# Performance work log

Hardware: AMD Instinct MI355X
Metric: run time of the kernel (lower is better)

## Reference

```python
import jax, jax.numpy as jnp
import numpy as np

NCLS = 21
HW = 41  # featUpsample target size


def setup_inputs() -> dict:
    key = jax.random.key(0)
    ks = jax.random.split(key, 8)
    x = jax.random.normal(ks[0], (4, 2048, 33, 33), dtype=jnp.float32)
    diffW = jax.random.uniform(ks[1], (4, HW * HW, HW * HW), dtype=jnp.float32)
    # conv weights init normal(0, 0.01) as in the torch module
    conv_w = jax.random.normal(ks[2], (1024, 2048, 3, 3), dtype=jnp.float32) * 0.01
    conv_b = jnp.zeros((1024,), jnp.float32)
    cls_w = jax.random.normal(ks[3], (NCLS, 1024, 1, 1), dtype=jnp.float32) * 0.01
    cls_b = jnp.zeros((NCLS,), jnp.float32)
    sm_scale_w = jnp.ones((1, NCLS), jnp.float32) * 1.5   # softMax_scale.weights
    pool_w = jnp.ones((1, NCLS), jnp.float32) * 5.0       # weiPooling.weights
    ms_scales = jnp.array([0.95, 0.75, 0.6, 0.4], jnp.float32)
    return {"x": x, "diffW": diffW, "conv_w": conv_w, "conv_b": conv_b,
            "cls_w": cls_w, "cls_b": cls_b, "sm_scale_w": sm_scale_w,
            "pool_w": pool_w, "ms_scales": ms_scales}


def reference(x, diffW, conv_w, conv_b, cls_w, cls_b, sm_scale_w, pool_w, ms_scales):
    bs = x.shape[0]
    # bilinear upsample to 41x41 (align_corners=False semantics, same as jax.image.resize)
    x = jax.image.resize(x, (bs, x.shape[1], HW, HW), method="bilinear")
    # ASPP branch 0: dilated 3x3 conv, dilation=padding=6 keeps 41x41
    feat = jax.lax.conv_general_dilated(
        x, conv_w, window_strides=(1, 1), padding=((6, 6), (6, 6)),
        rhs_dilation=(6, 6), dimension_numbers=("NCHW", "OIHW", "NCHW"))
    feat = feat + conv_b[None, :, None, None]          # [bs,1024,41,41]
    d = feat.shape[1]
    wh = HW * HW
    f2 = feat.reshape(bs, d, wh)                        # [bs,1024,wh]
    cw = cls_w.reshape(NCLS, d)                         # 1x1 conv weight

    logits = []
    for it in range(4):
        cs = (diffW > ms_scales[it]).astype(f2.dtype)   # [bs,wh,wh]
        # diag(1/rowsum) @ cs, then transpose -> column-normalized-after-transpose
        norm = (cs / cs.sum(axis=2, keepdims=True)).transpose(0, 2, 1)
        od = jnp.einsum("bdn,bnm->bdm", f2, norm)       # diffusion-smoothed features
        logits.append(jnp.einsum("bdm,cd->bcm", od, cw) + cls_b[None, :, None])
    wei_cum = jnp.stack(logits, axis=1)                 # [bs,4,ncls,wh]

    # softMax_scale: softmax over the scale (ns) axis of scaled logits
    wei_mask = jax.nn.softmax(sm_scale_w.reshape(1, 1, NCLS, 1) * wei_cum, axis=1)
    wei_cum2 = jax.nn.softmax((wei_cum * wei_mask).sum(axis=1), axis=1)  # [bs,ncls,wh]

    # weiPooling
    wei = jax.nn.softmax(wei_cum2, axis=1)
    w2 = jax.nn.softmax(wei * jnp.exp(pool_w[0]).reshape(1, NCLS, 1), axis=2)
    pooled = jnp.einsum("bcm,bdm->bcd", w2, f2)         # [bs,ncls,1024]

    # pred_sw with the 1x1 classifier weights
    out = (pooled * cw[None]).sum(axis=2) + cls_b[None]  # [bs,ncls]
    prob = jax.nn.sigmoid(out).reshape(bs, 1, NCLS)
    return (prob, wei_cum2, wei, wei_mask)
```

## Files before the change

### kernel.cpp

```cpp
#include <hip/hip_runtime.h>
#include <hip/hip_bf16.h>
#include <math.h>

#define NCLS 21
#define WH 1681
#define WHP 1684
#define BS 4
#define CIN 2048
#define NSRC 1089
#define KPOS 18432
#define MR 192
#define HS 836352
#define NT 53
#define NZ 8
#define PSLAB (16L * 22L * WHP)
#define MGK 16
#define MPOS 387072

typedef __attribute__((ext_vector_type(8))) __bf16 bf16x8;
typedef __attribute__((ext_vector_type(4))) float f32x4;

#define WS_W2M   0L
#define WS_KC    393216L
#define WS_H2    393248L
#define WS_WCUM  (WS_H2 + 4L * HS)
#define WS_G     (WS_WCUM + 564816L)
#define WS_GSW   (WS_G + 141204L)
#define WS_PACC0 (WS_GSW + 108544L)
#define WS_W2P   (WS_PACC0 + 591712L)
#define WS_W2MB  (WS_W2P + 6193152L)

static __device__ __forceinline__ unsigned short f2bf(float v) {
    unsigned int b = __float_as_uint(v);
    b += 0x7FFFu + ((b >> 16) & 1u);
    return (unsigned short)(b >> 16);
}


__global__ __launch_bounds__(128) void k_mergemm(const float* __restrict__ convw,
                                                 const float* __restrict__ clsw,
                                                 float* __restrict__ w2p) {
    int tid = threadIdx.x;
    int pos0 = blockIdx.x * 512 + tid * 4;
    int kz = blockIdx.y;
    int k0 = kz * 64;
    const float* cb = convw + (long)k0 * KPOS + pos0;

    float4 acc[21];
#pragma unroll
    for (int c = 0; c < 21; ++c) acc[c] = (float4){0.f, 0.f, 0.f, 0.f};

    float4 cur[4];
#pragma unroll
    for (int j = 0; j < 4; ++j) cur[j] = *(const float4*)(cb + (long)j * KPOS);

    for (int kk = 0; kk < 64; kk += 4) {
        float4 nxt[4];
        if (kk + 4 < 64) {
#pragma unroll
            for (int j = 0; j < 4; ++j) nxt[j] = *(const float4*)(cb + (long)(kk + 4 + j) * KPOS);
        }
        float4 cw[21];
#pragma unroll
        for (int c = 0; c < 21; ++c) cw[c] = *(const float4*)&clsw[c * 1024 + k0 + kk];
#pragma unroll
        for (int j = 0; j < 4; ++j) {
#pragma unroll
            for (int c = 0; c < 21; ++c) {
                float s = ((const float*)&cw[c])[j];
                acc[c].x += s * cur[j].x; acc[c].y += s * cur[j].y;
                acc[c].z += s * cur[j].z; acc[c].w += s * cur[j].w;
            }
        }
        if (kk + 4 < 64) {
#pragma unroll
            for (int j = 0; j < 4; ++j) cur[j] = nxt[j];
        }
    }
    float* op = w2p + (long)kz * MPOS + pos0;
#pragma unroll
    for (int c = 0; c < 21; ++c) *(float4*)(op + (long)c * KPOS) = acc[c];
}

__global__ void k_mfin(const float* __restrict__ w2p, float* __restrict__ w2m) {
    int gid = blockIdx.x * blockDim.x + threadIdx.x;
    if (gid >= MPOS) return;
    int r = gid / 2048;
    int i = gid - r * 2048;
    int c = r / 9, t = r - c * 9;
    long src = (long)c * KPOS + i * 9 + t;
    float s = 0.f;
#pragma unroll
    for (int kz = 0; kz < MGK; ++kz) s += w2p[(long)kz * MPOS + src];
    w2m[gid] = s;
}

__global__ void k_wpack(const float* __restrict__ w2m, unsigned short* __restrict__ w2mb) {
    int gid = blockIdx.x * blockDim.x + threadIdx.x;
    if (gid >= 64 * 12 * 64) return;
    int lane = gid & 63;
    int rt = (gid >> 6) % 12;
    int kc = gid / (64 * 12);
    int cl = lane & 15, kg = lane >> 4;
    const float* src = w2m + (long)(rt * 16 + cl) * 2048 + kc * 32 + kg * 8;
    unsigned short o[8];
#pragma unroll
    for (int j = 0; j < 8; ++j) o[j] = f2bf(src[j]);
    unsigned short* p = w2mb + (long)gid * 8;
#pragma unroll
    for (int j = 0; j < 8; ++j) p[j] = o[j];
}

__global__ void k_const(const float* __restrict__ clsw, const float* __restrict__ convb,
                        const float* __restrict__ clsb, float* __restrict__ Kc) {
    __shared__ float red[256];
    int c = blockIdx.x;
    float s = 0.f;
    for (int d = threadIdx.x; d < 1024; d += 256) s += clsw[c * 1024 + d] * convb[d];
    red[threadIdx.x] = s; __syncthreads();
    for (int o = 128; o > 0; o >>= 1) {
        if (threadIdx.x < o) red[threadIdx.x] += red[threadIdx.x + o];
        __syncthreads();
    }
    if (threadIdx.x == 0) Kc[c] = red[0] + clsb[c];
}

__global__ __launch_bounds__(256) void k_gemmm(const unsigned short* __restrict__ w2mb,
                                               const float* __restrict__ x,
                                               float* __restrict__ Hp) {
    __shared__ unsigned short Bs[2][64][40];
    int tid = threadIdx.x;
    int lane = tid & 63, wv = tid >> 6;
    int kg = lane >> 4, cl = lane & 15;
    int n0 = blockIdx.x * 64;
    int b  = blockIdx.y;
    int ks = blockIdx.z;

    const float* xb = x + ((long)b * CIN + ks * 512) * NSRC + n0 + lane;
    bool nok = (n0 + lane) < NSRC;

    f32x4 acc[3][4];
#pragma unroll
    for (int i = 0; i < 3; ++i)
#pragma unroll
        for (int ct = 0; ct < 4; ++ct) acc[i][ct] = (f32x4){0.f, 0.f, 0.f, 0.f};

    for (int ch = 0; ch < 16; ++ch) {
        const float* xc = xb + (long)(ch * 32 + wv * 8) * NSRC;
        float xr[8];
#pragma unroll
        for (int jj = 0; jj < 8; ++jj) xr[jj] = nok ? xc[(long)jj * NSRC] : 0.f;
        bf16x8 afr[3];
        const unsigned short* wb = w2mb + (((long)(ks * 16 + ch) * 12 + wv * 3) * 64 + lane) * 8;
#pragma unroll
        for (int i = 0; i < 3; ++i) afr[i] = *(const bf16x8*)(wb + (long)i * 64 * 8);
        union { unsigned short u[8]; bf16x8 v; } bw;
#pragma unroll
        for (int jj = 0; jj < 8; ++jj) bw.u[jj] = f2bf(xr[jj]);
        int buf = ch & 1;
        *(bf16x8*)&Bs[buf][lane][wv * 8] = bw.v;
        __syncthreads();
#pragma unroll
        for (int ct = 0; ct < 4; ++ct) {
            bf16x8 bf = *(const bf16x8*)&Bs[buf][ct * 16 + cl][kg * 8];
#pragma unroll
            for (int i = 0; i < 3; ++i)
                acc[i][ct] = __builtin_amdgcn_mfma_f32_16x16x32_bf16(afr[i], bf, acc[i][ct], 0, 0, 0);
        }
    }
    float* Hb = Hp + (long)ks * HS + (long)b * MR * NSRC;
#pragma unroll
    for (int i = 0; i < 3; ++i) {
        int r0 = (wv * 3 + i) * 16 + 4 * kg;
#pragma unroll
        for (int ct = 0; ct < 4; ++ct) {
            int n = n0 + ct * 16 + cl;
            if (n < NSRC) {
#pragma unroll
                for (int rr = 0; rr < 4; ++rr)
                    Hb[(long)(r0 + rr) * NSRC + n] = acc[i][ct][rr];
            }
        }
    }
}

__global__ void k_combine(const float* __restrict__ Hp, float* __restrict__ g) {
    int gid = blockIdx.x * blockDim.x + threadIdx.x;
    if (gid >= BS * NCLS * WH) return;
    int m = gid % WH;
    int t_ = gid / WH;
    int c = t_ % NCLS;
    int b = t_ / NCLS;
    int yy = m / 41, xx = m - yy * 41;
    const float S = 33.0f / 41.0f;
    int y0a[3], y1a[3], x0a[3], x1a[3];
    float wya[3], wxa[3];
    bool oky[3], okx[3];
#pragma unroll
    for (int o = 0; o < 3; ++o) {
        int yp = yy + 6 * o - 6;
        oky[o] = (yp >= 0 && yp < 41);
        float sy = (yp + 0.5f) * S - 0.5f;
        float fy = floorf(sy);
        wya[o] = sy - fy;
        int y0 = (int)fy;
        y0a[o] = min(max(y0, 0), 32);
        y1a[o] = min(max(y0 + 1, 0), 32);
        int xp = xx + 6 * o - 6;
        okx[o] = (xp >= 0 && xp < 41);
        float sx = (xp + 0.5f) * S - 0.5f;
        float fx = floorf(sx);
        wxa[o] = sx - fx;
        int x0 = (int)fx;
        x0a[o] = min(max(x0, 0), 32);
        x1a[o] = min(max(x0 + 1, 0), 32);
    }
    float acc = 0.f;
    const float* Hb = Hp + ((long)b * MR + c * 9) * NSRC;
#pragma unroll
    for (int ty = 0; ty < 3; ++ty) {
#pragma unroll
        for (int tx = 0; tx < 3; ++tx) {
            if (oky[ty] && okx[tx]) {
                const float* hr = Hb + (ty * 3 + tx) * NSRC;
                int i00 = y0a[ty] * 33 + x0a[tx], i01 = y0a[ty] * 33 + x1a[tx];
                int i10 = y1a[ty] * 33 + x0a[tx], i11 = y1a[ty] * 33 + x1a[tx];
                float v00 = 0.f, v01 = 0.f, v10 = 0.f, v11 = 0.f;
#pragma unroll
                for (int s = 0; s < 4; ++s) {
                    const float* h2 = hr + (long)s * HS;
                    v00 += h2[i00]; v01 += h2[i01]; v10 += h2[i10]; v11 += h2[i11];
                }
                float wy = wya[ty], wx = wxa[tx];
                float v0 = v00 + wx * (v01 - v00);
                float v1 = v10 + wx * (v11 - v10);
                acc += v0 + wy * (v1 - v0);
            }
        }
    }
    g[gid] = acc;
}

__global__ void k_gpack(const float* __restrict__ g, unsigned short* __restrict__ Gsw) {
    int gid = blockIdx.x * blockDim.x + threadIdx.x;
    if (gid >= BS * NT * 2 * 64) return;
    int lane = gid & 63;
    int t = gid >> 6;
    int ct = t & 1; t >>= 1;
    int nt = t % NT;
    int b  = t / NT;
    int col = ct * 16 + (lane & 15);
    int nb = nt * 32 + (lane >> 4) * 8;
    unsigned short out[8];
#pragma unroll
    for (int j = 0; j < 8; ++j) {
        int n = nb + j;
        unsigned short v = 0;
        if (n < WH) {
            if (col < NCLS) v = f2bf(g[((long)b * NCLS + col) * WH + n]);
            else if (col == NCLS) v = 0x3F80;
        }
        out[j] = v;
    }
    unsigned short* p = Gsw + (long)gid * 8;
#pragma unroll
    for (int j = 0; j < 8; ++j) p[j] = out[j];
}

__global__ __launch_bounds__(256) void k_dgemm(const float* __restrict__ diffW,
                                               const unsigned short* __restrict__ Gsw,
                                               const float* __restrict__ msc,
                                               float* __restrict__ pacc) {
    int tid  = threadIdx.x;
    int lane = tid & 63, wv = tid >> 6;
    int b = blockIdx.y, z = blockIdx.z;
    int m0w = blockIdx.x * 64 + wv * 16;
    int kg = lane >> 4;
    int cl = lane & 15;
    int mA = m0w + cl; if (mA > WH - 1) mA = WH - 1;
    float thr[4];
#pragma unroll
    for (int it = 0; it < 4; ++it) thr[it] = msc[it];
    int nt0 = (z * NT) / NZ;
    int nt1 = ((z + 1) * NT) / NZ;
    const float* drow = diffW + ((long)b * WH + mA) * WH;
    const unsigned short* gb = Gsw + (long)b * NT * 2 * 64 * 8;

    f32x4 accv[4][2];
#pragma unroll
    for (int it = 0; it < 4; ++it)
#pragma unroll
        for (int ct = 0; ct < 2; ++ct) accv[it][ct] = (f32x4){0.f, 0.f, 0.f, 0.f};

    for (int nt = nt0; nt < nt1; ++nt) {
        int nb = nt * 32 + kg * 8;
        float dw[8];
        if (nb + 7 <= WH - 1) {
#pragma unroll
            for (int j = 0; j < 8; ++j) dw[j] = drow[nb + j];
        } else {
#pragma unroll
            for (int j = 0; j < 8; ++j) dw[j] = (nb + j < WH) ? drow[nb + j] : -1e30f;
        }
        union { unsigned short u[8]; bf16x8 v; } af[4];
#pragma unroll
        for (int it = 0; it < 4; ++it)
#pragma unroll
            for (int j = 0; j < 8; ++j)
                af[it].u[j] = (dw[j] > thr[it]) ? (unsigned short)0x3F80 : (unsigned short)0;

        const unsigned short* gp = gb + ((long)nt * 2 * 64 + lane) * 8;
        bf16x8 b0 = *(const bf16x8*)gp;
        bf16x8 b1 = *(const bf16x8*)(gp + 64 * 8);
#pragma unroll
        for (int it = 0; it < 4; ++it) {
            accv[it][0] = __builtin_amdgcn_mfma_f32_16x16x32_bf16(af[it].v, b0, accv[it][0], 0, 0, 0);
            accv[it][1] = __builtin_amdgcn_mfma_f32_16x16x32_bf16(af[it].v, b1, accv[it][1], 0, 0, 0);
        }
    }
    float* pz = pacc + (long)z * PSLAB;
    int mbase = m0w + 4 * kg;
#pragma unroll
    for (int it = 0; it < 4; ++it) {
#pragma unroll
        for (int ct = 0; ct < 2; ++ct) {
            int c = ct * 16 + cl;
            if (c < 22) {
                float* dst = pz + ((long)(b * 4 + it) * 22 + c) * WHP + mbase;
                if (mbase + 3 < WH) {
                    *(f32x4*)dst = accv[it][ct];
                } else {
#pragma unroll
                    for (int r = 0; r < 4; ++r)
                        if (mbase + r < WH) dst[r] = accv[it][ct][r];
                }
            }
        }
    }
}

__global__ void k_dfin(const float* __restrict__ pacc, const float* __restrict__ Kc,
                       float* __restrict__ wcum) {
    int gid = blockIdx.x * blockDim.x + threadIdx.x;
    if (gid >= BS * 4 * NCLS * WH) return;
    int m = gid % WH;
    int t = gid / WH;
    int c = t % NCLS; t /= NCLS;
    int it = t & 3;
    int b = t >> 2;
    long rowc = ((long)(b * 4 + it) * 22 + c) * WHP + m;
    long rown = ((long)(b * 4 + it) * 22 + NCLS) * WHP + m;
    float num = 0.f, cnt = 0.f;
#pragma unroll
    for (int z = 0; z < NZ; ++z) {
        num += pacc[(long)z * PSLAB + rowc];
        cnt += pacc[(long)z * PSLAB + rown];
    }
    wcum[(((long)b * 4 + it) * NCLS + c) * WH + m] = num / cnt + Kc[c];
}

__global__ void k_mask(const float* __restrict__ wcum, const float* __restrict__ smw,
                       float* __restrict__ out_wc2, float* __restrict__ out_wei,
                       float* __restrict__ out_mask) {
    int gid = blockIdx.x * blockDim.x + threadIdx.x;
    if (gid >= BS * WH) return;
    int b = gid / WH, m = gid - b * WH;
    const float* base = wcum + (long)b * 4 * NCLS * WH + m;

    float fused[21];
#pragma unroll
    for (int c = 0; c < NCLS; ++c) {
        float sc = smw[c];
        float L0 = base[(0 * NCLS + c) * WH];
        float L1 = base[(1 * NCLS + c) * WH];
        float L2 = base[(2 * NCLS + c) * WH];
        float L3 = base[(3 * NCLS + c) * WH];
        float a0 = sc * L0, a1 = sc * L1, a2 = sc * L2, a3 = sc * L3;
        float mx = fmaxf(fmaxf(a0, a1), fmaxf(a2, a3));
        float e0 = __expf(a0 - mx), e1 = __expf(a1 - mx), e2 = __expf(a2 - mx), e3 = __expf(a3 - mx);
        float inv = 1.0f / (e0 + e1 + e2 + e3);
        e0 *= inv; e1 *= inv; e2 *= inv; e3 *= inv;
        out_mask[((long)(b * 4 + 0) * NCLS + c) * WH + m] = e0;
        out_mask[((long)(b * 4 + 1) * NCLS + c) * WH + m] = e1;
        out_mask[((long)(b * 4 + 2) * NCLS + c) * WH + m] = e2;
        out_mask[((long)(b * 4 + 3) * NCLS + c) * WH + m] = e3;
        fused[c] = L0 * e0 + L1 * e1 + L2 * e2 + L3 * e3;
    }
    float mx = -1e30f;
#pragma unroll
    for (int c = 0; c < NCLS; ++c) mx = fmaxf(mx, fused[c]);
    float s = 0.f;
    float e[21];
#pragma unroll
    for (int c = 0; c < NCLS; ++c) { e[c] = __expf(fused[c] - mx); s += e[c]; }
    float inv = 1.0f / s;
#pragma unroll
    for (int c = 0; c < NCLS; ++c) {
        e[c] *= inv;
        out_wc2[((long)b * NCLS + c) * WH + m] = e[c];
    }
    mx = -1e30f;
#pragma unroll
    for (int c = 0; c < NCLS; ++c) mx = fmaxf(mx, e[c]);
    s = 0.f;
    float e2a[21];
#pragma unroll
    for (int c = 0; c < NCLS; ++c) { e2a[c] = __expf(e[c] - mx); s += e2a[c]; }
    inv = 1.0f / s;
#pragma unroll
    for (int c = 0; c < NCLS; ++c) out_wei[((long)b * NCLS + c) * WH + m] = e2a[c] * inv;
}

__global__ void k_pool(const float* __restrict__ wei, const float* __restrict__ g,
                       const float* __restrict__ poolw, const float* __restrict__ Kc,
                       float* __restrict__ prob) {
    int c = blockIdx.x, b = blockIdx.y;
    const float* wr = wei + ((long)b * NCLS + c) * WH;
    const float* gr = g + ((long)b * NCLS + c) * WH;
    float E = __expf(poolw[c]);
    __shared__ float red[256];
    float mx = -1e30f;
    for (int m = threadIdx.x; m < WH; m += 256) mx = fmaxf(mx, wr[m] * E);
    red[threadIdx.x] = mx; __syncthreads();
    for (int o = 128; o > 0; o >>= 1) {
        if (threadIdx.x < o) red[threadIdx.x] = fmaxf(red[threadIdx.x], red[threadIdx.x + o]);
        __syncthreads();
    }
    mx = red[0]; __syncthreads();
    float se = 0.f, sg = 0.f;
    for (int m = threadIdx.x; m < WH; m += 256) {
        float ev = __expf(wr[m] * E - mx);
        se += ev; sg += ev * gr[m];
    }
    red[threadIdx.x] = se; __syncthreads();
    for (int o = 128; o > 0; o >>= 1) {
        if (threadIdx.x < o) red[threadIdx.x] += red[threadIdx.x + o];
        __syncthreads();
    }
    se = red[0]; __syncthreads();
    red[threadIdx.x] = sg; __syncthreads();
    for (int o = 128; o > 0; o >>= 1) {
        if (threadIdx.x < o) red[threadIdx.x] += red[threadIdx.x + o];
        __syncthreads();
    }
    sg = red[0];
    if (threadIdx.x == 0) {
        float out = sg / se + Kc[c];
        prob[b * NCLS + c] = 1.0f / (1.0f + __expf(-out));
    }
}

extern "C" void kernel_launch(void* const* d_in, const int* in_sizes, int n_in,
                              void* d_out, int out_size, void* d_ws, size_t ws_size,
                              hipStream_t stream) {
    const float* x      = (const float*)d_in[0];
    const float* diffW  = (const float*)d_in[1];
    const float* conv_w = (const float*)d_in[2];
    const float* conv_b = (const float*)d_in[3];
    const float* cls_w  = (const float*)d_in[4];
    const float* cls_b  = (const float*)d_in[5];
    const float* smw    = (const float*)d_in[6];
    const float* poolw  = (const float*)d_in[7];
    const float* msc    = (const float*)d_in[8];

    float* ws   = (float*)d_ws;
    float* w2m  = ws + WS_W2M;
    float* Kc   = ws + WS_KC;
    float* Hp   = ws + WS_H2;
    float* wcum = ws + WS_WCUM;
    float* g    = ws + WS_G;
    unsigned short* Gsw  = (unsigned short*)(ws + WS_GSW);
    float* w2p  = ws + WS_W2P;
    float* pacc = ws + WS_W2P;
    unsigned short* w2mb = (unsigned short*)(ws + WS_W2MB);

    float* out  = (float*)d_out;
    float* o_prob = out;
    float* o_wc2  = out + 84;
    float* o_wei  = out + 84 + 141204;
    float* o_mask = out + 84 + 141204 + 141204;

    hipMemsetAsync(w2m, 0, 393216 * sizeof(float), stream);

    k_mergemm<<<dim3(36, MGK), 128, 0, stream>>>(conv_w, cls_w, w2p);
    k_mfin<<<(MPOS + 255) / 256, 256, 0, stream>>>(w2p, w2m);
    k_wpack<<<(64 * 12 * 64 + 255) / 256, 256, 0, stream>>>(w2m, w2mb);
    k_const<<<NCLS, 256, 0, stream>>>(cls_w, conv_b, cls_b, Kc);
    k_gemmm<<<dim3(18, BS, 4), 256, 0, stream>>>(w2mb, x, Hp);
    k_combine<<<(BS * NCLS * WH + 255) / 256, 256, 0, stream>>>(Hp, g);
    k_gpack<<<(BS * NT * 2 * 64 + 255) / 256, 256, 0, stream>>>(g, Gsw);
    k_dgemm<<<dim3(27, BS, NZ), 256, 0, stream>>>(diffW, Gsw, msc, pacc);
    k_dfin<<<(BS * 4 * NCLS * WH + 255) / 256, 256, 0, stream>>>(pacc, Kc, wcum);
    k_mask<<<(BS * WH + 255) / 256, 256, 0, stream>>>(wcum, smw, o_wc2, o_wei, o_mask);
    k_pool<<<dim3(NCLS, BS), 256, 0, stream>>>(o_wei, g, poolw, Kc, o_prob);
}
```

Baseline: 113.5 us.

## Compute merged classifier-conv weights with bf16 MFMA and fuse reduce+pack

The fp32 FMA kernel that multiplies the classifier weights into the conv weights is replaced by a bf16 MFMA kernel, fed by a new pre-pack of the classifier weights. The split-K depth drops from 16 to 4 slices, and the separate finalize and pack kernels plus a memset become one reduce-and-pack kernel. This targets the preprocessing cost of streaming the large conv weight tensor and the extra launches. It adds bf16 rounding at an earlier stage, and a trailing __syncthreads is also inserted in k_gemmm's loop.

After: 98.90 us. -12.9%, faster.

```diff
diff --git a/kernel.cpp b/kernel.cpp
--- a/kernel.cpp
+++ b/kernel.cpp
@@ -14,20 +14,19 @@
 #define NT 53
 #define NZ 8
 #define PSLAB (16L * 22L * WHP)
-#define MGK 16
-#define MPOS 387072
+#define MKZ 4
+#define MSLAB (32L * KPOS)
 
 typedef __attribute__((ext_vector_type(8))) __bf16 bf16x8;
 typedef __attribute__((ext_vector_type(4))) float f32x4;
 
-#define WS_W2M   0L
 #define WS_KC    393216L
 #define WS_H2    393248L
 #define WS_WCUM  (WS_H2 + 4L * HS)
 #define WS_G     (WS_WCUM + 564816L)
 #define WS_GSW   (WS_G + 141204L)
-#define WS_PACC0 (WS_GSW + 108544L)
-#define WS_W2P   (WS_PACC0 + 591712L)
+#define WS_CF    (WS_GSW + 108544L)
+#define WS_W2P   (WS_CF + 591712L)
 #define WS_W2MB  (WS_W2P + 6193152L)
 
 static __device__ __forceinline__ unsigned short f2bf(float v) {
@@ -37,75 +36,99 @@
 }
 
 
-__global__ __launch_bounds__(128) void k_mergemm(const float* __restrict__ convw,
-                                                 const float* __restrict__ clsw,
-                                                 float* __restrict__ w2p) {
+__global__ void k_cpack(const float* __restrict__ clsw, unsigned short* __restrict__ cf) {
+    int gid = blockIdx.x * blockDim.x + threadIdx.x;
+    if (gid >= 32 * 2 * 64) return;
+    int lane = gid & 63;
+    int rt = (gid >> 6) & 1;
+    int kc = gid >> 7;
+    int cl = lane & 15, kg = lane >> 4;
+    int c = rt * 16 + cl;
+    unsigned short o[8];
+#pragma unroll
+    for (int j = 0; j < 8; ++j) {
+        int d = kc * 32 + kg * 8 + j;
+        o[j] = (c < NCLS) ? f2bf(clsw[c * 1024 + d]) : (unsigned short)0;
+    }
+    unsigned short* p = cf + (long)gid * 8;
+#pragma unroll
+    for (int j = 0; j < 8; ++j) p[j] = o[j];
+}
+
+__global__ __launch_bounds__(256) void k_mergemm(const unsigned short* __restrict__ cf,
+                                                 const float* __restrict__ convw,
+                                                 float* __restrict__ pmrg) {
+    __shared__ unsigned short Bs[2][64][40];
     int tid = threadIdx.x;
-    int pos0 = blockIdx.x * 512 + tid * 4;
+    int lane = tid & 63, wv = tid >> 6;
+    int kg = lane >> 4, cl = lane & 15;
+    int pos0 = blockIdx.x * 64;
     int kz = blockIdx.y;
-    int k0 = kz * 64;
-    const float* cb = convw + (long)k0 * KPOS + pos0;
-
-    float4 acc[21];
-#pragma unroll
-    for (int c = 0; c < 21; ++c) acc[c] = (float4){0.f, 0.f, 0.f, 0.f};
-
-    float4 cur[4];
-#pragma unroll
-    for (int j = 0; j < 4; ++j) cur[j] = *(const float4*)(cb + (long)j * KPOS);
-
-    for (int kk = 0; kk < 64; kk += 4) {
-        float4 nxt[4];
-        if (kk + 4 < 64) {
-#pragma unroll
-            for (int j = 0; j < 4; ++j) nxt[j] = *(const float4*)(cb + (long)(kk + 4 + j) * KPOS);
-        }
-        float4 cw[21];
-#pragma unroll
-        for (int c = 0; c < 21; ++c) cw[c] = *(const float4*)&clsw[c * 1024 + k0 + kk];
-#pragma unroll
-        for (int j = 0; j < 4; ++j) {
-#pragma unroll
-            for (int c = 0; c < 21; ++c) {
-                float s = ((const float*)&cw[c])[j];
-                acc[c].x += s * cur[j].x; acc[c].y += s * cur[j].y;
-                acc[c].z += s * cur[j].z; acc[c].w += s * cur[j].w;
-            }
-        }
-        if (kk + 4 < 64) {
-#pragma unroll
-            for (int j = 0; j < 4; ++j) cur[j] = nxt[j];
-        }
-    }
-    float* op = w2p + (long)kz * MPOS + pos0;
-#pragma unroll
-    for (int c = 0; c < 21; ++c) *(float4*)(op + (long)c * KPOS) = acc[c];
-}
-
-__global__ void k_mfin(const float* __restrict__ w2p, float* __restrict__ w2m) {
-    int gid = blockIdx.x * blockDim.x + threadIdx.x;
-    if (gid >= MPOS) return;
-    int r = gid / 2048;
-    int i = gid - r * 2048;
-    int c = r / 9, t = r - c * 9;
-    long src = (long)c * KPOS + i * 9 + t;
-    float s = 0.f;
-#pragma unroll
-    for (int kz = 0; kz < MGK; ++kz) s += w2p[(long)kz * MPOS + src];
-    w2m[gid] = s;
-}
-
-__global__ void k_wpack(const float* __restrict__ w2m, unsigned short* __restrict__ w2mb) {
+
+    const float* cb = convw + (long)(kz * 256) * KPOS + pos0 + lane;
+
+    f32x4 acc[2];
+#pragma unroll
+    for (int i = 0; i < 2; ++i) acc[i] = (f32x4){0.f, 0.f, 0.f, 0.f};
+
+    for (int ch = 0; ch < 8; ++ch) {
+        const float* cc = cb + (long)(ch * 32 + wv * 8) * KPOS;
+        float xr[8];
+#pragma unroll
+        for (int jj = 0; jj < 8; ++jj) xr[jj] = cc[(long)jj * KPOS];
+        bf16x8 afr[2];
+        const unsigned short* ab = cf + (((long)(kz * 8 + ch) * 2) * 64 + lane) * 8;
+#pragma unroll
+        for (int i = 0; i < 2; ++i) afr[i] = *(const bf16x8*)(ab + (long)i * 64 * 8);
+        union { unsigned short u[8]; bf16x8 v; } bw;
+#pragma unroll
+        for (int jj = 0; jj < 8; ++jj) bw.u[jj] = f2bf(xr[jj]);
+        int buf = ch & 1;
+        *(bf16x8*)&Bs[buf][lane][wv * 8] = bw.v;
+        __syncthreads();
+        bf16x8 bf = *(const bf16x8*)&Bs[buf][wv * 16 + cl][kg * 8];
+#pragma unroll
+        for (int i = 0; i < 2; ++i)
+            acc[i] = __builtin_amdgcn_mfma_f32_16x16x32_bf16(afr[i], bf, acc[i], 0, 0, 0);
+        __syncthreads();
+    }
+    float* pz = pmrg + (long)kz * MSLAB;
+    int pos = pos0 + wv * 16 + cl;
+#pragma unroll
+    for (int i = 0; i < 2; ++i) {
+#pragma unroll
+        for (int rr = 0; rr < 4; ++rr) {
+            int c = i * 16 + 4 * kg + rr;
+            pz[(long)c * KPOS + pos] = acc[i][rr];
+        }
+    }
+}
+
+__global__ void k_mfinpack(const float* __restrict__ pmrg, unsigned short* __restrict__ w2mb) {
     int gid = blockIdx.x * blockDim.x + threadIdx.x;
     if (gid >= 64 * 12 * 64) return;
     int lane = gid & 63;
     int rt = (gid >> 6) % 12;
     int kc = gid / (64 * 12);
     int cl = lane & 15, kg = lane >> 4;
-    const float* src = w2m + (long)(rt * 16 + cl) * 2048 + kc * 32 + kg * 8;
+    int r = rt * 16 + cl;
     unsigned short o[8];
-#pragma unroll
-    for (int j = 0; j < 8; ++j) o[j] = f2bf(src[j]);
+    if (r < 189) {
+        int c = r / 9, t = r - c * 9;
+        const float* base = pmrg + (long)c * KPOS + t;
+#pragma unroll
+        for (int j = 0; j < 8; ++j) {
+            int i = kc * 32 + kg * 8 + j;
+            long pos = (long)i * 9;
+            float s = 0.f;
+#pragma unroll
+            for (int kz = 0; kz < MKZ; ++kz) s += base[(long)kz * MSLAB + pos];
+            o[j] = f2bf(s);
+        }
+    } else {
+#pragma unroll
+        for (int j = 0; j < 8; ++j) o[j] = 0;
+    }
     unsigned short* p = w2mb + (long)gid * 8;
 #pragma unroll
     for (int j = 0; j < 8; ++j) p[j] = o[j];
@@ -167,6 +190,7 @@
             for (int i = 0; i < 3; ++i)
                 acc[i][ct] = __builtin_amdgcn_mfma_f32_16x16x32_bf16(afr[i], bf, acc[i][ct], 0, 0, 0);
         }
+        __syncthreads();
     }
     float* Hb = Hp + (long)ks * HS + (long)b * MR * NSRC;
 #pragma unroll
@@ -464,13 +488,13 @@
     const float* msc    = (const float*)d_in[8];
 
     float* ws   = (float*)d_ws;
-    float* w2m  = ws + WS_W2M;
     float* Kc   = ws + WS_KC;
     float* Hp   = ws + WS_H2;
     float* wcum = ws + WS_WCUM;
     float* g    = ws + WS_G;
     unsigned short* Gsw  = (unsigned short*)(ws + WS_GSW);
-    float* w2p  = ws + WS_W2P;
+    unsigned short* cf   = (unsigned short*)(ws + WS_CF);
+    float* pmrg = ws + WS_W2P;
     float* pacc = ws + WS_W2P;
     unsigned short* w2mb = (unsigned short*)(ws + WS_W2MB);
 
@@ -480,11 +504,9 @@
     float* o_wei  = out + 84 + 141204;
     float* o_mask = out + 84 + 141204 + 141204;
 
-    hipMemsetAsync(w2m, 0, 393216 * sizeof(float), stream);
-
-    k_mergemm<<<dim3(36, MGK), 128, 0, stream>>>(conv_w, cls_w, w2p);
-    k_mfin<<<(MPOS + 255) / 256, 256, 0, stream>>>(w2p, w2m);
-    k_wpack<<<(64 * 12 * 64 + 255) / 256, 256, 0, stream>>>(w2m, w2mb);
+    k_cpack<<<(32 * 2 * 64 + 255) / 256, 256, 0, stream>>>(cls_w, cf);
+    k_mergemm<<<dim3(KPOS / 64, MKZ), 256, 0, stream>>>(cf, conv_w, pmrg);
+    k_mfinpack<<<(64 * 12 * 64 + 255) / 256, 256, 0, stream>>>(pmrg, w2mb);
     k_const<<<NCLS, 256, 0, stream>>>(cls_w, conv_b, cls_b, Kc);
     k_gemmm<<<dim3(18, BS, 4), 256, 0, stream>>>(w2mb, x, Hp);
     k_combine<<<(BS * NCLS * WH + 255) / 256, 256, 0, stream>>>(Hp, g);
```
